# Kernel tuning notes

Hardware: AMD Instinct MI355X
Metric: run time of the kernel (lower is better)

## Reference

```python
import jax, jax.numpy as jnp
import numpy as np

N_HEAD = 16

def setup_inputs() -> dict:
    key = jax.random.key(0)
    k1, k2, k3 = jax.random.split(key, 3)
    C = 1024
    x = jax.random.normal(k1, (2, 2048, C), dtype=jnp.float32)
    W_attn = jax.random.normal(k2, (C, 3 * C), dtype=jnp.float32) * (C ** -0.5)
    b_attn = jnp.zeros((3 * C,), dtype=jnp.float32)
    W_proj = jax.random.normal(k3, (C, C), dtype=jnp.float32) * (C ** -0.5)
    b_proj = jnp.zeros((C,), dtype=jnp.float32)
    return {"x": x, "W_attn": W_attn, "b_attn": b_attn, "W_proj": W_proj, "b_proj": b_proj}

def reference(x, W_attn, b_attn, W_proj, b_proj):
    B, T, C = x.shape
    H = N_HEAD
    hd = C // H
    qkv = x @ W_attn + b_attn                      # [B,T,3C]
    q, k, v = jnp.split(qkv, 3, axis=-1)
    q = q.reshape(B, T, H, hd).transpose(0, 2, 1, 3)  # [B,H,T,hd]
    k = k.reshape(B, T, H, hd).transpose(0, 2, 1, 3)
    v = v.reshape(B, T, H, hd).transpose(0, 2, 1, 3)
    att = jnp.einsum('bhqd,bhkd->bhqk', q, k) * (1.0 / jnp.sqrt(jnp.float32(hd)))
    causal = jnp.tril(jnp.ones((T, T), dtype=bool))
    att = jnp.where(causal[None, None, :, :], att, jnp.float32(-jnp.inf))
    att = jax.nn.softmax(att, axis=-1)
    y = jnp.einsum('bhqk,bhkd->bhqd', att, v)       # [B,H,T,hd]
    y = y.transpose(0, 2, 1, 3).reshape(B, T, C)
    return y @ W_proj + b_proj
```

## Files before the change

### kernel.cpp

```cpp
#include <hip/hip_runtime.h>
#include <hip/hip_bf16.h>

typedef unsigned short u16;
using frag_ab = __attribute__((ext_vector_type(8))) short;
using f32x4   = __attribute__((ext_vector_type(4))) float;
using u16x4   = __attribute__((ext_vector_type(4))) unsigned short;
using u16x8   = __attribute__((ext_vector_type(8))) unsigned short;

#define N_CTX   2048
#define NBATCH  2
#define CDIM    1024
#define NH      16
#define HD      64

__device__ __forceinline__ u16 f2b(float f) {
  __hip_bfloat16 h = __float2bfloat16(f);
  return __builtin_bit_cast(u16, h);
}

__device__ __forceinline__ f32x4 mfma16(frag_ab a, frag_ab b, f32x4 c) {
  return __builtin_amdgcn_mfma_f32_16x16x32_bf16(a, b, c, 0, 0, 0);
}

#define GLDS16(src, dst) \
  __builtin_amdgcn_global_load_lds((const __attribute__((address_space(1))) void*)(src), \
                                   (__attribute__((address_space(3))) void*)(dst), 16, 0, 0)

__global__ __launch_bounds__(256) void cvt_f32_bf16(const float* __restrict__ in,
                                                    u16* __restrict__ out, int n8) {
  int i = blockIdx.x * 256 + threadIdx.x;
  if (i >= n8) return;
  const f32x4* ip = (const f32x4*)in;
  f32x4 a = ip[2 * i], b2 = ip[2 * i + 1];
  u16x8 r;
  #pragma unroll
  for (int j = 0; j < 4; ++j) { r[j] = f2b(a[j]); r[4 + j] = f2b(b2[j]); }
  ((u16x8*)out)[i] = r;
}

__global__ __launch_bounds__(256) void transpose_cvt(const float* __restrict__ in,
                                                     u16* __restrict__ out, int K, int N) {
  __shared__ float tile[32][33];
  int n0 = blockIdx.x * 32, k0 = blockIdx.y * 32;
  int c = threadIdx.x & 31, r0 = threadIdx.x >> 5;
  #pragma unroll
  for (int i = 0; i < 4; ++i) {
    int r = r0 + i * 8;
    tile[r][c] = in[(size_t)(k0 + r) * N + n0 + c];
  }
  __syncthreads();
  #pragma unroll
  for (int i = 0; i < 4; ++i) {
    int r = r0 + i * 8;
    out[(size_t)(n0 + r) * K + k0 + c] = f2b(tile[c][r]);
  }
}

__global__ __launch_bounds__(512, 4) void gemm_qkv128(const u16* __restrict__ A,
                                                      const u16* __restrict__ Bt,
                                                      const float* __restrict__ bias,
                                                      u16* __restrict__ Qo, u16* __restrict__ Ko,
                                                      u16* __restrict__ Vto) {
  __shared__ __align__(16) u16 As[2][128 * 64];
  __shared__ __align__(16) u16 Bs[2][192 * 64];
  const int tid = threadIdx.x, w = tid >> 6, lane = tid & 63;
  const int g = lane >> 4, lr = lane & 15;
  const int wr = w >> 2, wc = w & 3;
  const int bid = blockIdx.x;
  const int swz = (bid & 7) * 64 + (bid >> 3);
  const int tm = (swz & 31) * 128, tn = (swz >> 5) * 192;

  f32x4 acc[4][3];
  #pragma unroll
  for (int mi = 0; mi < 4; ++mi)
    #pragma unroll
    for (int ni = 0; ni < 3; ++ni)
      acc[mi][ni] = (f32x4){0.f, 0.f, 0.f, 0.f};

  auto STAGE = [&](int d, int kt) {
    const int k0 = kt << 6;
    #pragma unroll
    for (int j = 0; j < 2; ++j) {
      int ci = j * 512 + tid, row = ci >> 3, c8 = ci & 7;
      GLDS16(A + (size_t)(tm + row) * CDIM + k0 + ((c8 ^ (row & 7)) << 3),
             &As[d][row * 64 + c8 * 8]);
    }
    #pragma unroll
    for (int j = 0; j < 3; ++j) {
      int ci = j * 512 + tid, row = ci >> 3, c8 = ci & 7;
      GLDS16(Bt + (size_t)(tn + row) * CDIM + k0 + ((c8 ^ (row & 7)) << 3),
             &Bs[d][row * 64 + c8 * 8]);
    }
  };

  STAGE(0, 0);
  asm volatile("s_waitcnt vmcnt(0)" ::: "memory");
  __builtin_amdgcn_s_barrier();

  const int x7 = lr & 7;
  for (int t = 0; t < 16; ++t) {
    const int cur = t & 1;
    if (t < 15) STAGE(cur ^ 1, t + 1);

    frag_ab af[4][2], bf[3][2];
    #pragma unroll
    for (int mi = 0; mi < 4; ++mi) {
      int row = wr * 64 + mi * 16 + lr;
      #pragma unroll
      for (int ks = 0; ks < 2; ++ks)
        af[mi][ks] = *(const frag_ab*)&As[cur][row * 64 + ((((ks << 2) | g) ^ x7) << 3)];
    }
    #pragma unroll
    for (int ni = 0; ni < 3; ++ni) {
      int row = wc * 48 + ni * 16 + lr;
      #pragma unroll
      for (int ks = 0; ks < 2; ++ks)
        bf[ni][ks] = *(const frag_ab*)&Bs[cur][row * 64 + ((((ks << 2) | g) ^ x7) << 3)];
    }
    __builtin_amdgcn_s_setprio(1);
    #pragma unroll
    for (int mi = 0; mi < 4; ++mi)
      #pragma unroll
      for (int ni = 0; ni < 3; ++ni)
        #pragma unroll
        for (int ks = 0; ks < 2; ++ks)
          acc[mi][ni] = mfma16(af[mi][ks], bf[ni][ks], acc[mi][ni]);
    __builtin_amdgcn_s_setprio(0);

    asm volatile("s_waitcnt vmcnt(0)" ::: "memory");
    __builtin_amdgcn_s_barrier();
  }

  #pragma unroll
  for (int ni = 0; ni < 3; ++ni) {
    int n = tn + wc * 48 + ni * 16 + lr;
    float bv = bias[n];
    int which = n >> 10, c = n & 1023, h = c >> 6, d = c & 63;
    #pragma unroll
    for (int mi = 0; mi < 4; ++mi) {
      if (which == 2) {
        int t0 = tm + wr * 64 + mi * 16 + g * 4;
        int bb = t0 >> 11, tt = t0 & (N_CTX - 1);
        u16x4 pk;
        #pragma unroll
        for (int r = 0; r < 4; ++r) pk[r] = f2b(acc[mi][ni][r] + bv);
        *(u16x4*)&Vto[((size_t)(bb * NH + h) * HD + d) * N_CTX + tt] = pk;
      } else {
        u16* dst = (which == 0) ? Qo : Ko;
        float scl = (which == 0) ? 0.180336881f : 1.0f;
        #pragma unroll
        for (int r = 0; r < 4; ++r) {
          int m = tm + wr * 64 + mi * 16 + g * 4 + r;
          int bb = m >> 11, tt = m & (N_CTX - 1);
          dst[((size_t)(bb * NH + h) * N_CTX + tt) * HD + d] = f2b((acc[mi][ni][r] + bv) * scl);
        }
      }
    }
  }
}

__global__ __launch_bounds__(512, 4) void gemm_proj128(const u16* __restrict__ A,
                                                       const u16* __restrict__ Bt,
                                                       const float* __restrict__ bias,
                                                       float* __restrict__ out) {
  __shared__ __align__(16) u16 As[2][128 * 64];
  __shared__ __align__(16) u16 Bs[2][64 * 64];
  const int tid = threadIdx.x, w = tid >> 6, lane = tid & 63;
  const int g = lane >> 4, lr = lane & 15;
  const int wr = w >> 1, wc = w & 1;
  const int bid = blockIdx.x;
  const int swz = (bid & 7) * 64 + (bid >> 3);
  const int tm = (swz & 31) * 128, tn = (swz >> 5) * 64;

  f32x4 acc[2][2];
  #pragma unroll
  for (int mi = 0; mi < 2; ++mi)
    #pragma unroll
    for (int ni = 0; ni < 2; ++ni)
      acc[mi][ni] = (f32x4){0.f, 0.f, 0.f, 0.f};

  auto STAGE = [&](int d, int kt) {
    const int k0 = kt << 6;
    #pragma unroll
    for (int j = 0; j < 2; ++j) {
      int ci = j * 512 + tid, row = ci >> 3, c8 = ci & 7;
      GLDS16(A + (size_t)(tm + row) * CDIM + k0 + ((c8 ^ (row & 7)) << 3),
             &As[d][row * 64 + c8 * 8]);
    }
    {
      int row = tid >> 3, c8 = tid & 7;
      GLDS16(Bt + (size_t)(tn + row) * CDIM + k0 + ((c8 ^ (row & 7)) << 3),
             &Bs[d][row * 64 + c8 * 8]);
    }
  };

  STAGE(0, 0);
  asm volatile("s_waitcnt vmcnt(0)" ::: "memory");
  __builtin_amdgcn_s_barrier();

  const int x7 = lr & 7;
  for (int t = 0; t < 16; ++t) {
    const int cur = t & 1;
    if (t < 15) STAGE(cur ^ 1, t + 1);

    frag_ab af[2][2], bf[2][2];
    #pragma unroll
    for (int mi = 0; mi < 2; ++mi) {
      int row = wr * 32 + mi * 16 + lr;
      #pragma unroll
      for (int ks = 0; ks < 2; ++ks)
        af[mi][ks] = *(const frag_ab*)&As[cur][row * 64 + ((((ks << 2) | g) ^ x7) << 3)];
    }
    #pragma unroll
    for (int ni = 0; ni < 2; ++ni) {
      int row = wc * 32 + ni * 16 + lr;
      #pragma unroll
      for (int ks = 0; ks < 2; ++ks)
        bf[ni][ks] = *(const frag_ab*)&Bs[cur][row * 64 + ((((ks << 2) | g) ^ x7) << 3)];
    }
    __builtin_amdgcn_s_setprio(1);
    #pragma unroll
    for (int mi = 0; mi < 2; ++mi)
      #pragma unroll
      for (int ni = 0; ni < 2; ++ni)
        #pragma unroll
        for (int ks = 0; ks < 2; ++ks)
          acc[mi][ni] = mfma16(af[mi][ks], bf[ni][ks], acc[mi][ni]);
    __builtin_amdgcn_s_setprio(0);

    asm volatile("s_waitcnt vmcnt(0)" ::: "memory");
    __builtin_amdgcn_s_barrier();
  }

  #pragma unroll
  for (int ni = 0; ni < 2; ++ni) {
    int n = tn + wc * 32 + ni * 16 + lr;
    float bv = bias[n];
    #pragma unroll
    for (int mi = 0; mi < 2; ++mi)
      #pragma unroll
      for (int r = 0; r < 4; ++r) {
        int m = tm + wr * 32 + mi * 16 + g * 4 + r;
        out[(size_t)m * CDIM + n] = acc[mi][ni][r] + bv;
      }
  }
}

__global__ __launch_bounds__(256, 2) void attn_fwd(const u16* __restrict__ Q, const u16* __restrict__ K,
                                                   const u16* __restrict__ Vt, u16* __restrict__ Y) {
  __shared__ __align__(16) u16 Ks[4][64 * 64];
  __shared__ __align__(16) u16 Vs[4][64 * 64];
  const int orig = blockIdx.x;
  const int swz = (orig & 7) * 64 + (orig >> 3);
  const int bh = swz >> 4;
  const int p  = swz & 15;
  const int qta = p, qtb = 31 - p;
  const int tid = threadIdx.x, w = tid >> 6, lane = tid & 63;
  const int g = lane >> 4, lr = lane & 15;
  const size_t base = (size_t)bh * N_CTX * HD;
  const u16* Kbh = K + base;
  const u16* Vbh = Vt + base;

  const int c8 = tid & 7;
  const int row0 = tid >> 3;
  const int row1 = row0 + 32;
  const size_t kOff0 = (size_t)row0 * HD + (size_t)((c8 ^ (row0 & 7)) * 8);
  const size_t kOff1 = (size_t)row1 * HD + (size_t)((c8 ^ (row1 & 7)) * 8);
  const size_t vOff0 = (size_t)row0 * N_CTX + (size_t)((c8 ^ (row0 & 7)) * 8);
  const size_t vOff1 = (size_t)row1 * N_CTX + (size_t)((c8 ^ (row1 & 7)) * 8);

  frag_ab qfA[2], qfB[2];
  {
    const u16* qa = Q + base + (size_t)(qta * 64 + w * 16 + lr) * HD + g * 8;
    qfA[0] = *(const frag_ab*)qa;  qfA[1] = *(const frag_ab*)(qa + 32);
    const u16* qb = Q + base + (size_t)(qtb * 64 + w * 16 + lr) * HD + g * 8;
    qfB[0] = *(const frag_ab*)qb;  qfB[1] = *(const frag_ab*)(qb + 32);
  }

  float psA = 0.f, psB = 0.f;
  f32x4 oA[4], oB[4];
  #pragma unroll
  for (int d = 0; d < 4; ++d) { oA[d] = (f32x4){0,0,0,0}; oB[d] = (f32x4){0,0,0,0}; }

  auto STAGE = [&](int b, int kt) {
    const u16* ks = Kbh + (size_t)kt * 64 * HD;
    const u16* vs = Vbh + (size_t)kt * 64;
    GLDS16(ks + kOff0, &Ks[b][(size_t)tid * 8]);
    GLDS16(ks + kOff1, &Ks[b][(size_t)(tid + 256) * 8]);
    GLDS16(vs + vOff0, &Vs[b][(size_t)tid * 8]);
    GLDS16(vs + vOff1, &Vs[b][(size_t)(tid + 256) * 8]);
  };

  frag_ab vfl[4][4];

  auto softmax_pv = [&](f32x4 (&s)[8], f32x4 (&o)[4], float& ps, int d0, int d1) {
    const int qrow = w * 16 + lr;
    if (d0 == 0) {
      #pragma unroll
      for (int nf = 0; nf < 4; ++nf)
        #pragma unroll
        for (int r = 0; r < 4; ++r)
          if (nf * 16 + g * 4 + r > qrow) s[nf][r] = -1e30f;
    }
    if (d1 >= 0) {
      const int off = d1 * 64;
      #pragma unroll
      for (int nf = 0; nf < 4; ++nf)
        #pragma unroll
        for (int r = 0; r < 4; ++r)
          if (off + nf * 16 + g * 4 + r > qrow) s[4 + nf][r] = -1e30f;
    }
    #pragma unroll
    for (int j = 0; j < 8; ++j)
      #pragma unroll
      for (int r = 0; r < 4; ++r)
        s[j][r] = __builtin_amdgcn_exp2f(s[j][r]);
    float ts[8];
    #pragma unroll
    for (int j = 0; j < 8; ++j)
      ts[j] = (s[j][0] + s[j][1]) + (s[j][2] + s[j][3]);
    ps += ((ts[0] + ts[1]) + (ts[2] + ts[3])) + ((ts[4] + ts[5]) + (ts[6] + ts[7]));
    frag_ab pa[4];
    #pragma unroll
    for (int ks = 0; ks < 4; ++ks)
      #pragma unroll
      for (int j = 0; j < 4; ++j) {
        pa[ks][j]     = (short)f2b(s[2 * ks][j]);
        pa[ks][4 + j] = (short)f2b(s[2 * ks + 1][j]);
      }
    __builtin_amdgcn_s_setprio(1);
    #pragma unroll
    for (int d = 0; d < 4; ++d)
      #pragma unroll
      for (int ks = 0; ks < 4; ++ks)
        o[d] = mfma16(pa[ks], vfl[d][ks], o[d]);
    __builtin_amdgcn_s_setprio(0);
  };

  const int npair = (qtb + 2) >> 1;
  STAGE(0, 0);
  STAGE(1, 1);
  asm volatile("s_waitcnt vmcnt(0)" ::: "memory");
  __builtin_amdgcn_s_barrier();

  for (int i = 0; i < npair; ++i) {
    const int t0 = 2 * i, t1 = 2 * i + 1;
    const int b0 = t0 & 3, b1 = t1 & 3;
    if (i + 1 < npair) { STAGE((t0 + 2) & 3, t0 + 2); STAGE((t1 + 2) & 3, t1 + 2); }

    frag_ab kf[8][2];
    #pragma unroll
    for (int nf = 0; nf < 4; ++nf)
      #pragma unroll
      for (int ks = 0; ks < 2; ++ks) {
        kf[nf][ks]     = *(const frag_ab*)&Ks[b0][(size_t)(nf * 16 + lr) * 64 +
                                                  (size_t)((((ks << 2) | g) ^ (lr & 7)) * 8)];
        kf[4 + nf][ks] = *(const frag_ab*)&Ks[b1][(size_t)(nf * 16 + lr) * 64 +
                                                  (size_t)((((ks << 2) | g) ^ (lr & 7)) * 8)];
      }

    const bool aAct = (t0 <= qta);
    const bool aT1  = (t1 <= qta);

    f32x4 sB[8], sA[8];
    __builtin_amdgcn_s_setprio(1);
    #pragma unroll
    for (int j = 0; j < 8; ++j) {
      f32x4 a = (f32x4){0.f, 0.f, 0.f, 0.f};
      a = mfma16(kf[j][0], qfB[0], a);
      a = mfma16(kf[j][1], qfB[1], a);
      sB[j] = a;
    }
    if (aAct) {
      #pragma unroll
      for (int j = 0; j < 4; ++j) {
        f32x4 a = (f32x4){0.f, 0.f, 0.f, 0.f};
        a = mfma16(kf[j][0], qfA[0], a);
        a = mfma16(kf[j][1], qfA[1], a);
        sA[j] = a;
      }
      if (aT1) {
        #pragma unroll
        for (int j = 4; j < 8; ++j) {
          f32x4 a = (f32x4){0.f, 0.f, 0.f, 0.f};
          a = mfma16(kf[j][0], qfA[0], a);
          a = mfma16(kf[j][1], qfA[1], a);
          sA[j] = a;
        }
      } else {
        #pragma unroll
        for (int j = 4; j < 8; ++j)
          sA[j] = (f32x4){-1e30f, -1e30f, -1e30f, -1e30f};
      }
    }
    __builtin_amdgcn_s_setprio(0);

    #pragma unroll
    for (int d = 0; d < 4; ++d) {
      const int row = (d * 16 + lr) * 64;
      #pragma unroll
      for (int ks = 0; ks < 2; ++ks) {
        u16x4 lo0 = *(const u16x4*)&Vs[b0][row + (((ks * 4 + (g >> 1)) ^ (lr & 7)) * 8) + (g & 1) * 4];
        u16x4 hi0 = *(const u16x4*)&Vs[b0][row + (((ks * 4 + 2 + (g >> 1)) ^ (lr & 7)) * 8) + (g & 1) * 4];
        u16x4 lo1 = *(const u16x4*)&Vs[b1][row + (((ks * 4 + (g >> 1)) ^ (lr & 7)) * 8) + (g & 1) * 4];
        u16x4 hi1 = *(const u16x4*)&Vs[b1][row + (((ks * 4 + 2 + (g >> 1)) ^ (lr & 7)) * 8) + (g & 1) * 4];
        frag_ab v0, v1;
        #pragma unroll
        for (int j = 0; j < 4; ++j) {
          v0[j] = (short)lo0[j];  v0[4 + j] = (short)hi0[j];
          v1[j] = (short)lo1[j];  v1[4 + j] = (short)hi1[j];
        }
        vfl[d][ks]     = v0;
        vfl[d][2 + ks] = v1;
      }
    }

    softmax_pv(sB, oB, psB, t0 - qtb, t1 - qtb);
    if (aAct) softmax_pv(sA, oA, psA, t0 - qta, t1 - qta);

    asm volatile("s_waitcnt vmcnt(0)" ::: "memory");
    __builtin_amdgcn_s_barrier();
  }

  const int b = bh >> 4, h = bh & 15;
  float sumA = psA, sumB = psB;
  sumA += __shfl_xor(sumA, 16, 64);  sumA += __shfl_xor(sumA, 32, 64);
  sumB += __shfl_xor(sumB, 16, 64);  sumB += __shfl_xor(sumB, 32, 64);
  float liA = 1.0f / sumA, liB = 1.0f / sumB;
  #pragma unroll
  for (int r = 0; r < 4; ++r) {
    int src = (lane & 48) | (((lane >> 4) & 3) * 4 + r);
    float lA = __shfl(liA, src, 64);
    float lB = __shfl(liB, src, 64);
    int rowA = qta * 64 + w * 16 + g * 4 + r;
    int rowB = qtb * 64 + w * 16 + g * 4 + r;
    #pragma unroll
    for (int d = 0; d < 4; ++d) {
      Y[((size_t)(b * N_CTX + rowA)) * CDIM + h * HD + d * 16 + lr] = f2b(oA[d][r] * lA);
      Y[((size_t)(b * N_CTX + rowB)) * CDIM + h * HD + d * 16 + lr] = f2b(oB[d][r] * lB);
    }
  }
}

extern "C" void kernel_launch(void* const* d_in, const int* in_sizes, int n_in,
                              void* d_out, int out_size, void* d_ws, size_t ws_size,
                              hipStream_t stream) {
  const float* x      = (const float*)d_in[0];
  const float* W_attn = (const float*)d_in[1];
  const float* b_attn = (const float*)d_in[2];
  const float* W_proj = (const float*)d_in[3];
  const float* b_proj = (const float*)d_in[4];
  float* out = (float*)d_out;
  char* ws = (char*)d_ws;

  u16* xb  = (u16*)(ws);
  u16* Wab = (u16*)(ws + ((size_t)8 << 20));
  u16* Wpb = (u16*)(ws + ((size_t)14 << 20));
  u16* Qb  = (u16*)(ws + ((size_t)16 << 20));
  u16* Kb  = (u16*)(ws + ((size_t)24 << 20));
  u16* Vtb = (u16*)(ws + ((size_t)32 << 20));
  u16* yb  = xb;

  cvt_f32_bf16<<<2048, 256, 0, stream>>>(x, xb, (NBATCH * N_CTX * CDIM) / 8);
  transpose_cvt<<<dim3(3 * CDIM / 32, CDIM / 32), 256, 0, stream>>>(W_attn, Wab, CDIM, 3 * CDIM);
  transpose_cvt<<<dim3(CDIM / 32, CDIM / 32), 256, 0, stream>>>(W_proj, Wpb, CDIM, CDIM);
  gemm_qkv128<<<512, 512, 0, stream>>>(xb, Wab, b_attn, Qb, Kb, Vtb);
  attn_fwd<<<512, 256, 0, stream>>>(Qb, Kb, Vtb, yb);
  gemm_proj128<<<512, 512, 0, stream>>>(yb, Wpb, b_proj, out);
}
```

Baseline: 102.1 us.

## Split attention query-tile pair across two wave groups and fuse prep kernels

The attention kernel now runs 512 threads per block. Each group of four waves handles one of the two paired causal query tiles, instead of each wave processing both tiles serially. K/V staging is shared across all 512 threads, so each thread issues one load per tile instead of two. The lighter-loaded group skips inactive tiles but still joins the barriers. Separately, the three fp32-to-bf16 preparation kernels are merged into one launch to cut launch overhead. The split raises parallelism and cuts per-wave register use, at the cost of imbalance between the two groups inside a block.

New measurement: 91.75 us. 1.11x faster.

```diff
diff --git a/kernel.cpp b/kernel.cpp
--- a/kernel.cpp
+++ b/kernel.cpp
@@ -26,22 +26,30 @@
   __builtin_amdgcn_global_load_lds((const __attribute__((address_space(1))) void*)(src), \
                                    (__attribute__((address_space(3))) void*)(dst), 16, 0, 0)
 
-__global__ __launch_bounds__(256) void cvt_f32_bf16(const float* __restrict__ in,
-                                                    u16* __restrict__ out, int n8) {
-  int i = blockIdx.x * 256 + threadIdx.x;
-  if (i >= n8) return;
-  const f32x4* ip = (const f32x4*)in;
-  f32x4 a = ip[2 * i], b2 = ip[2 * i + 1];
-  u16x8 r;
-  #pragma unroll
-  for (int j = 0; j < 4; ++j) { r[j] = f2b(a[j]); r[4 + j] = f2b(b2[j]); }
-  ((u16x8*)out)[i] = r;
-}
-
-__global__ __launch_bounds__(256) void transpose_cvt(const float* __restrict__ in,
-                                                     u16* __restrict__ out, int K, int N) {
+__global__ __launch_bounds__(256) void prep_all(const float* __restrict__ x, u16* __restrict__ xb,
+                                                const float* __restrict__ Wa, u16* __restrict__ Wab,
+                                                const float* __restrict__ Wp, u16* __restrict__ Wpb) {
   __shared__ float tile[32][33];
-  int n0 = blockIdx.x * 32, k0 = blockIdx.y * 32;
+  const int blk = blockIdx.x;
+  if (blk < 2048) {
+    int i = blk * 256 + threadIdx.x;
+    const f32x4* ip = (const f32x4*)x;
+    f32x4 a = ip[2 * i], b2 = ip[2 * i + 1];
+    u16x8 r;
+    #pragma unroll
+    for (int j = 0; j < 4; ++j) { r[j] = f2b(a[j]); r[4 + j] = f2b(b2[j]); }
+    ((u16x8*)xb)[i] = r;
+    return;
+  }
+  const float* in; u16* out; int K, N, bx, by;
+  if (blk < 5120) {
+    int idx = blk - 2048; in = Wa; out = Wab; K = CDIM; N = 3 * CDIM;
+    bx = idx % 96; by = idx / 96;
+  } else {
+    int idx = blk - 5120; in = Wp; out = Wpb; K = CDIM; N = CDIM;
+    bx = idx & 31; by = idx >> 5;
+  }
+  int n0 = bx * 32, k0 = by * 32;
   int c = threadIdx.x & 31, r0 = threadIdx.x >> 5;
   #pragma unroll
   for (int i = 0; i < 4; ++i) {
@@ -246,7 +254,7 @@
   }
 }
 
-__global__ __launch_bounds__(256, 2) void attn_fwd(const u16* __restrict__ Q, const u16* __restrict__ K,
+__global__ __launch_bounds__(512, 4) void attn_fwd(const u16* __restrict__ Q, const u16* __restrict__ K,
                                                    const u16* __restrict__ Vt, u16* __restrict__ Y) {
   __shared__ __align__(16) u16 Ks[4][64 * 64];
   __shared__ __align__(16) u16 Vs[4][64 * 64];
@@ -254,87 +262,33 @@
   const int swz = (orig & 7) * 64 + (orig >> 3);
   const int bh = swz >> 4;
   const int p  = swz & 15;
-  const int qta = p, qtb = 31 - p;
+  const int qtb = 31 - p;
   const int tid = threadIdx.x, w = tid >> 6, lane = tid & 63;
+  const int grp = w >> 2, wq = w & 3;
+  const int qt  = grp ? qtb : p;
   const int g = lane >> 4, lr = lane & 15;
   const size_t base = (size_t)bh * N_CTX * HD;
   const u16* Kbh = K + base;
   const u16* Vbh = Vt + base;
 
-  const int c8 = tid & 7;
-  const int row0 = tid >> 3;
-  const int row1 = row0 + 32;
-  const size_t kOff0 = (size_t)row0 * HD + (size_t)((c8 ^ (row0 & 7)) * 8);
-  const size_t kOff1 = (size_t)row1 * HD + (size_t)((c8 ^ (row1 & 7)) * 8);
-  const size_t vOff0 = (size_t)row0 * N_CTX + (size_t)((c8 ^ (row0 & 7)) * 8);
-  const size_t vOff1 = (size_t)row1 * N_CTX + (size_t)((c8 ^ (row1 & 7)) * 8);
-
-  frag_ab qfA[2], qfB[2];
+  const int c8 = tid & 7, srow = tid >> 3;
+  const size_t kOff = (size_t)srow * HD + (size_t)((c8 ^ (srow & 7)) * 8);
+  const size_t vOff = (size_t)srow * N_CTX + (size_t)((c8 ^ (srow & 7)) * 8);
+
+  frag_ab qf[2];
   {
-    const u16* qa = Q + base + (size_t)(qta * 64 + w * 16 + lr) * HD + g * 8;
-    qfA[0] = *(const frag_ab*)qa;  qfA[1] = *(const frag_ab*)(qa + 32);
-    const u16* qb = Q + base + (size_t)(qtb * 64 + w * 16 + lr) * HD + g * 8;
-    qfB[0] = *(const frag_ab*)qb;  qfB[1] = *(const frag_ab*)(qb + 32);
-  }
-
-  float psA = 0.f, psB = 0.f;
-  f32x4 oA[4], oB[4];
-  #pragma unroll
-  for (int d = 0; d < 4; ++d) { oA[d] = (f32x4){0,0,0,0}; oB[d] = (f32x4){0,0,0,0}; }
+    const u16* qp = Q + base + (size_t)(qt * 64 + wq * 16 + lr) * HD + g * 8;
+    qf[0] = *(const frag_ab*)qp;  qf[1] = *(const frag_ab*)(qp + 32);
+  }
+
+  float ps = 0.f;
+  f32x4 o[4];
+  #pragma unroll
+  for (int d = 0; d < 4; ++d) o[d] = (f32x4){0.f, 0.f, 0.f, 0.f};
 
   auto STAGE = [&](int b, int kt) {
-    const u16* ks = Kbh + (size_t)kt * 64 * HD;
-    const u16* vs = Vbh + (size_t)kt * 64;
-    GLDS16(ks + kOff0, &Ks[b][(size_t)tid * 8]);
-    GLDS16(ks + kOff1, &Ks[b][(size_t)(tid + 256) * 8]);
-    GLDS16(vs + vOff0, &Vs[b][(size_t)tid * 8]);
-    GLDS16(vs + vOff1, &Vs[b][(size_t)(tid + 256) * 8]);
-  };
-
-  frag_ab vfl[4][4];
-
-  auto softmax_pv = [&](f32x4 (&s)[8], f32x4 (&o)[4], float& ps, int d0, int d1) {
-    const int qrow = w * 16 + lr;
-    if (d0 == 0) {
-      #pragma unroll
-      for (int nf = 0; nf < 4; ++nf)
-        #pragma unroll
-        for (int r = 0; r < 4; ++r)
-          if (nf * 16 + g * 4 + r > qrow) s[nf][r] = -1e30f;
-    }
-    if (d1 >= 0) {
-      const int off = d1 * 64;
-      #pragma unroll
-      for (int nf = 0; nf < 4; ++nf)
-        #pragma unroll
-        for (int r = 0; r < 4; ++r)
-          if (off + nf * 16 + g * 4 + r > qrow) s[4 + nf][r] = -1e30f;
-    }
-    #pragma unroll
-    for (int j = 0; j < 8; ++j)
-      #pragma unroll
-      for (int r = 0; r < 4; ++r)
-        s[j][r] = __builtin_amdgcn_exp2f(s[j][r]);
-    float ts[8];
-    #pragma unroll
-    for (int j = 0; j < 8; ++j)
-      ts[j] = (s[j][0] + s[j][1]) + (s[j][2] + s[j][3]);
-    ps += ((ts[0] + ts[1]) + (ts[2] + ts[3])) + ((ts[4] + ts[5]) + (ts[6] + ts[7]));
-    frag_ab pa[4];
-    #pragma unroll
-    for (int ks = 0; ks < 4; ++ks)
-      #pragma unroll
-      for (int j = 0; j < 4; ++j) {
-        pa[ks][j]     = (short)f2b(s[2 * ks][j]);
-        pa[ks][4 + j] = (short)f2b(s[2 * ks + 1][j]);
-      }
-    __builtin_amdgcn_s_setprio(1);
-    #pragma unroll
-    for (int d = 0; d < 4; ++d)
-      #pragma unroll
-      for (int ks = 0; ks < 4; ++ks)
-        o[d] = mfma16(pa[ks], vfl[d][ks], o[d]);
-    __builtin_amdgcn_s_setprio(0);
+    GLDS16(Kbh + (size_t)kt * 64 * HD + kOff, &Ks[b][(size_t)tid * 8]);
+    GLDS16(Vbh + (size_t)kt * 64 + vOff,      &Vs[b][(size_t)tid * 8]);
   };
 
   const int npair = (qtb + 2) >> 1;
@@ -348,97 +302,102 @@
     const int b0 = t0 & 3, b1 = t1 & 3;
     if (i + 1 < npair) { STAGE((t0 + 2) & 3, t0 + 2); STAGE((t1 + 2) & 3, t1 + 2); }
 
-    frag_ab kf[8][2];
-    #pragma unroll
-    for (int nf = 0; nf < 4; ++nf)
-      #pragma unroll
-      for (int ks = 0; ks < 2; ++ks) {
-        kf[nf][ks]     = *(const frag_ab*)&Ks[b0][(size_t)(nf * 16 + lr) * 64 +
-                                                  (size_t)((((ks << 2) | g) ^ (lr & 7)) * 8)];
-        kf[4 + nf][ks] = *(const frag_ab*)&Ks[b1][(size_t)(nf * 16 + lr) * 64 +
-                                                  (size_t)((((ks << 2) | g) ^ (lr & 7)) * 8)];
-      }
-
-    const bool aAct = (t0 <= qta);
-    const bool aT1  = (t1 <= qta);
-
-    f32x4 sB[8], sA[8];
-    __builtin_amdgcn_s_setprio(1);
-    #pragma unroll
-    for (int j = 0; j < 8; ++j) {
-      f32x4 a = (f32x4){0.f, 0.f, 0.f, 0.f};
-      a = mfma16(kf[j][0], qfB[0], a);
-      a = mfma16(kf[j][1], qfB[1], a);
-      sB[j] = a;
-    }
-    if (aAct) {
-      #pragma unroll
-      for (int j = 0; j < 4; ++j) {
+    if (t0 <= qt) {
+      frag_ab kf[8][2];
+      #pragma unroll
+      for (int nf = 0; nf < 4; ++nf)
+        #pragma unroll
+        for (int ks = 0; ks < 2; ++ks) {
+          kf[nf][ks]     = *(const frag_ab*)&Ks[b0][(size_t)(nf * 16 + lr) * 64 +
+                                                    (size_t)((((ks << 2) | g) ^ (lr & 7)) * 8)];
+          kf[4 + nf][ks] = *(const frag_ab*)&Ks[b1][(size_t)(nf * 16 + lr) * 64 +
+                                                    (size_t)((((ks << 2) | g) ^ (lr & 7)) * 8)];
+        }
+      f32x4 s[8];
+      __builtin_amdgcn_s_setprio(1);
+      #pragma unroll
+      for (int j = 0; j < 8; ++j) {
         f32x4 a = (f32x4){0.f, 0.f, 0.f, 0.f};
-        a = mfma16(kf[j][0], qfA[0], a);
-        a = mfma16(kf[j][1], qfA[1], a);
-        sA[j] = a;
-      }
-      if (aT1) {
-        #pragma unroll
-        for (int j = 4; j < 8; ++j) {
-          f32x4 a = (f32x4){0.f, 0.f, 0.f, 0.f};
-          a = mfma16(kf[j][0], qfA[0], a);
-          a = mfma16(kf[j][1], qfA[1], a);
-          sA[j] = a;
+        a = mfma16(kf[j][0], qf[0], a);
+        a = mfma16(kf[j][1], qf[1], a);
+        s[j] = a;
+      }
+      __builtin_amdgcn_s_setprio(0);
+      const int qrow = wq * 16 + lr;
+      if (t0 == qt) {
+        #pragma unroll
+        for (int nf = 0; nf < 4; ++nf)
+          #pragma unroll
+          for (int r = 0; r < 4; ++r)
+            if (nf * 16 + g * 4 + r > qrow) s[nf][r] = -1e30f;
+      }
+      if (t1 >= qt) {
+        const int off = (t1 - qt) * 64;
+        #pragma unroll
+        for (int nf = 0; nf < 4; ++nf)
+          #pragma unroll
+          for (int r = 0; r < 4; ++r)
+            if (off + nf * 16 + g * 4 + r > qrow) s[4 + nf][r] = -1e30f;
+      }
+      #pragma unroll
+      for (int j = 0; j < 8; ++j)
+        #pragma unroll
+        for (int r = 0; r < 4; ++r)
+          s[j][r] = __builtin_amdgcn_exp2f(s[j][r]);
+      float ts[8];
+      #pragma unroll
+      for (int j = 0; j < 8; ++j)
+        ts[j] = (s[j][0] + s[j][1]) + (s[j][2] + s[j][3]);
+      ps += ((ts[0] + ts[1]) + (ts[2] + ts[3])) + ((ts[4] + ts[5]) + (ts[6] + ts[7]));
+      frag_ab pa[4];
+      #pragma unroll
+      for (int ks = 0; ks < 4; ++ks)
+        #pragma unroll
+        for (int j = 0; j < 4; ++j) {
+          pa[ks][j]     = (short)f2b(s[2 * ks][j]);
+          pa[ks][4 + j] = (short)f2b(s[2 * ks + 1][j]);
         }
-      } else {
-        #pragma unroll
-        for (int j = 4; j < 8; ++j)
-          sA[j] = (f32x4){-1e30f, -1e30f, -1e30f, -1e30f};
-      }
-    }
-    __builtin_amdgcn_s_setprio(0);
-
-    #pragma unroll
-    for (int d = 0; d < 4; ++d) {
-      const int row = (d * 16 + lr) * 64;
-      #pragma unroll
-      for (int ks = 0; ks < 2; ++ks) {
-        u16x4 lo0 = *(const u16x4*)&Vs[b0][row + (((ks * 4 + (g >> 1)) ^ (lr & 7)) * 8) + (g & 1) * 4];
-        u16x4 hi0 = *(const u16x4*)&Vs[b0][row + (((ks * 4 + 2 + (g >> 1)) ^ (lr & 7)) * 8) + (g & 1) * 4];
-        u16x4 lo1 = *(const u16x4*)&Vs[b1][row + (((ks * 4 + (g >> 1)) ^ (lr & 7)) * 8) + (g & 1) * 4];
-        u16x4 hi1 = *(const u16x4*)&Vs[b1][row + (((ks * 4 + 2 + (g >> 1)) ^ (lr & 7)) * 8) + (g & 1) * 4];
-        frag_ab v0, v1;
-        #pragma unroll
-        for (int j = 0; j < 4; ++j) {
-          v0[j] = (short)lo0[j];  v0[4 + j] = (short)hi0[j];
-          v1[j] = (short)lo1[j];  v1[4 + j] = (short)hi1[j];
+      #pragma unroll
+      for (int d = 0; d < 4; ++d) {
+        const int row = (d * 16 + lr) * 64;
+        frag_ab vf[4];
+        #pragma unroll
+        for (int ks = 0; ks < 2; ++ks) {
+          u16x4 lo0 = *(const u16x4*)&Vs[b0][row + (((ks * 4 + (g >> 1)) ^ (lr & 7)) * 8) + (g & 1) * 4];
+          u16x4 hi0 = *(const u16x4*)&Vs[b0][row + (((ks * 4 + 2 + (g >> 1)) ^ (lr & 7)) * 8) + (g & 1) * 4];
+          u16x4 lo1 = *(const u16x4*)&Vs[b1][row + (((ks * 4 + (g >> 1)) ^ (lr & 7)) * 8) + (g & 1) * 4];
+          u16x4 hi1 = *(const u16x4*)&Vs[b1][row + (((ks * 4 + 2 + (g >> 1)) ^ (lr & 7)) * 8) + (g & 1) * 4];
+          #pragma unroll
+          for (int j = 0; j < 4; ++j) {
+            vf[ks][j] = (short)lo0[j];      vf[ks][4 + j] = (short)hi0[j];
+            vf[2 + ks][j] = (short)lo1[j];  vf[2 + ks][4 + j] = (short)hi1[j];
+          }
         }
-        vfl[d][ks]     = v0;
-        vfl[d][2 + ks] = v1;
-      }
-    }
-
-    softmax_pv(sB, oB, psB, t0 - qtb, t1 - qtb);
-    if (aAct) softmax_pv(sA, oA, psA, t0 - qta, t1 - qta);
+        __builtin_amdgcn_s_setprio(1);
+        #pragma unroll
+        for (int ks = 0; ks < 4; ++ks)
+          o[d] = mfma16(pa[ks], vf[ks], o[d]);
+        __builtin_amdgcn_s_setprio(0);
+      }
+    }
 
     asm volatile("s_waitcnt vmcnt(0)" ::: "memory");
     __builtin_amdgcn_s_barrier();
   }
 
   const int b = bh >> 4, h = bh & 15;
-  float sumA = psA, sumB = psB;
-  sumA += __shfl_xor(sumA, 16, 64);  sumA += __shfl_xor(sumA, 32, 64);
-  sumB += __shfl_xor(sumB, 16, 64);  sumB += __shfl_xor(sumB, 32, 64);
-  float liA = 1.0f / sumA, liB = 1.0f / sumB;
+  float sum = ps;
+  sum += __shfl_xor(sum, 16, 64);
+  sum += __shfl_xor(sum, 32, 64);
+  float li = 1.0f / sum;
   #pragma unroll
   for (int r = 0; r < 4; ++r) {
     int src = (lane & 48) | (((lane >> 4) & 3) * 4 + r);
-    float lA = __shfl(liA, src, 64);
-    float lB = __shfl(liB, src, 64);
-    int rowA = qta * 64 + w * 16 + g * 4 + r;
-    int rowB = qtb * 64 + w * 16 + g * 4 + r;
-    #pragma unroll
-    for (int d = 0; d < 4; ++d) {
-      Y[((size_t)(b * N_CTX + rowA)) * CDIM + h * HD + d * 16 + lr] = f2b(oA[d][r] * lA);
-      Y[((size_t)(b * N_CTX + rowB)) * CDIM + h * HD + d * 16 + lr] = f2b(oB[d][r] * lB);
-    }
+    float lir = __shfl(li, src, 64);
+    int row = qt * 64 + wq * 16 + g * 4 + r;
+    #pragma unroll
+    for (int d = 0; d < 4; ++d)
+      Y[((size_t)(b * N_CTX + row)) * CDIM + h * HD + d * 16 + lr] = f2b(o[d][r] * lir);
   }
 }
 
@@ -461,10 +420,8 @@
   u16* Vtb = (u16*)(ws + ((size_t)32 << 20));
   u16* yb  = xb;
 
-  cvt_f32_bf16<<<2048, 256, 0, stream>>>(x, xb, (NBATCH * N_CTX * CDIM) / 8);
-  transpose_cvt<<<dim3(3 * CDIM / 32, CDIM / 32), 256, 0, stream>>>(W_attn, Wab, CDIM, 3 * CDIM);
-  transpose_cvt<<<dim3(CDIM / 32, CDIM / 32), 256, 0, stream>>>(W_proj, Wpb, CDIM, CDIM);
+  prep_all<<<6144, 256, 0, stream>>>(x, xb, W_attn, Wab, W_proj, Wpb);
   gemm_qkv128<<<512, 512, 0, stream>>>(xb, Wab, b_attn, Qb, Kb, Vtb);
-  attn_fwd<<<512, 256, 0, stream>>>(Qb, Kb, Vtb, yb);
+  attn_fwd<<<512, 512, 0, stream>>>(Qb, Kb, Vtb, yb);
   gemm_proj128<<<512, 512, 0, stream>>>(yb, Wpb, b_proj, out);
 }
```
